# Kernel tuning notes

Hardware: AMD Instinct MI355X
Metric: run time of the kernel (lower is better)

## Reference

```python
import jax, jax.numpy as jnp
import numpy as np

# ---- module hyperparams (match init_kwargs) ----
REGIONS_DIMS = [0, 1, 2, 4, 9, 16]
ALL_DIM = sum(REGIONS_DIMS)          # 32
NUM_REGIONS = len(REGIONS_DIMS)      # 6
FIELD_NUM = 32
VOCAB = 200000
BATCH = 8192
TEMPERATURE = 1.0
EPS = 1e-5                            # torch BatchNorm1d default eps


def _build_region_mask():
    """Replicates init_variables(): row 0 is all-zero (drop-feature region),
    rows 1..R-1 are disjoint consecutive segments of sizes REGIONS_DIMS[1:]."""
    mask = np.zeros((NUM_REGIONS, ALL_DIM), dtype=np.float32)
    dims_pre_sum = [0] + [sum(REGIONS_DIMS[1:i]) for i in range(2, NUM_REGIONS)]
    for r, (pre, dim) in enumerate(zip(dims_pre_sum, REGIONS_DIMS[1:]), start=1):
        mask[r, pre:pre + dim] = 1.0
    return jnp.asarray(mask)


def setup_inputs() -> dict:
    key = jax.random.key(0)
    k_ids, k_emb, k_w = jax.random.split(key, 3)
    input_ids = jax.random.randint(k_ids, (BATCH, FIELD_NUM), 0, VOCAB, dtype=jnp.int64)
    # torch.nn.init.uniform_(a=-0.05, b=0.05)
    emb_table = jax.random.uniform(k_emb, (VOCAB, ALL_DIM), dtype=jnp.float32,
                                   minval=-0.05, maxval=0.05)
    # xavier_uniform on [F, R, 1]: bound = sqrt(6/(R+1))
    bound = float(np.sqrt(6.0 / (NUM_REGIONS + 1)))
    field_region_weights = jax.random.uniform(
        k_w, (FIELD_NUM, NUM_REGIONS, 1), dtype=jnp.float32, minval=-bound, maxval=bound)
    return {
        "input_ids": input_ids,
        "emb_table": emb_table,
        "field_region_weights": field_region_weights,
        "region_mask": _build_region_mask(),
    }


def reference(input_ids, emb_table, field_region_weights, region_mask):
    # Embedding gather: [B, F, D]
    emb = emb_table[input_ids]
    # BatchNorm1d(field_num, affine=False), training mode: per-field stats over (batch, D),
    # biased variance (torch normalizes with biased var).
    mean = jnp.mean(emb, axis=(0, 2), keepdims=True)
    var = jnp.var(emb, axis=(0, 2), keepdims=True)
    x = (emb - mean) * jax.lax.rsqrt(var + EPS)
    # softmax over regions: [F, R]
    w = jax.nn.softmax(field_region_weights[..., 0] / TEMPERATURE, axis=1)
    # sum_r w[f,r] * mask[r,d] -> per-(field, dim) scale; equivalent to the original's
    # broadcast-to-[B,F,R,D], multiply, and sum over R, without the big intermediate.
    coef = jnp.einsum('fr,rd->fd', w, region_mask)
    return x * coef[None, :, :]
```

## Files before the change

kernel.cpp:

```cpp
#include <hip/hip_runtime.h>
#include <math.h>

#define BATCH    8192
#define FIELDS   32
#define DIM      32
#define NREG     6
#define EPS      1e-5f
#define NBLKA    4096
#define PBASE    64
#define SCALE_F  (PBASE + 64 * NBLKA)
#define BIAS_F   (SCALE_F + FIELDS * DIM)


__global__ __launch_bounds__(256) void irazor_stage_stats_kernel(
        const int*   __restrict__ ids,
        const float* __restrict__ table,
        float*       __restrict__ ws,
        float*       __restrict__ out) {
    const int t   = threadIdx.x;
    const int blk = blockIdx.x;
    const int f   = t >> 3;
    const int vec = t & 7;

    float4* __restrict__ out4 = reinterpret_cast<float4*>(out);
    float s = 0.f, sq = 0.f;
    #pragma unroll
    for (int i = 0; i < 2; ++i) {
        const int id = ids[(blk * 2 + i) * FIELDS + f];
        const float4 v = *reinterpret_cast<const float4*>(
            table + (size_t)id * DIM + vec * 4);
        out4[(size_t)blk * 512 + (size_t)i * 256 + t] = v;
        s  += v.x + v.y + v.z + v.w;
        sq += v.x * v.x + v.y * v.y + v.z * v.z + v.w * v.w;
    }

    #pragma unroll
    for (int off = 1; off < 8; off <<= 1) {
        s  += __shfl_xor(s, off);
        sq += __shfl_xor(sq, off);
    }
    if (vec == 0) {
        ws[PBASE + f * NBLKA + blk]        = s;
        ws[PBASE + (32 + f) * NBLKA + blk] = sq;
    }
}

__global__ __launch_bounds__(256) void irazor_finalize_kernel(
        const float* __restrict__ frw,
        const float* __restrict__ mask,
        float*       __restrict__ ws) {
    const int fld = blockIdx.x;
    const int t   = threadIdx.x;

    const float* __restrict__ ps = ws + PBASE + (size_t)fld * NBLKA;
    const float* __restrict__ pq = ws + PBASE + (size_t)(32 + fld) * NBLKA;
    float a = 0.f, b = 0.f;
    #pragma unroll
    for (int i = 0; i < NBLKA / 256; ++i) {
        a += ps[i * 256 + t];
        b += pq[i * 256 + t];
    }
    #pragma unroll
    for (int off = 1; off < 64; off <<= 1) {
        a += __shfl_xor(a, off);
        b += __shfl_xor(b, off);
    }
    __shared__ float ls[4], lq[4];
    const int wave = t >> 6;
    if ((t & 63) == 0) { ls[wave] = a; lq[wave] = b; }
    __syncthreads();
    const float S  = ls[0] + ls[1] + ls[2] + ls[3];
    const float SQ = lq[0] + lq[1] + lq[2] + lq[3];

    if (t < DIM) {
        const float invN = 1.f / (float)(BATCH * DIM);
        const float mean = S * invN;
        const float var  = SQ * invN - mean * mean;
        const float istd = rsqrtf(var + EPS);

        float w[NREG]; float m = -1e30f;
        #pragma unroll
        for (int r = 0; r < NREG; ++r) { w[r] = frw[fld * NREG + r]; m = fmaxf(m, w[r]); }
        float ssum = 0.f;
        #pragma unroll
        for (int r = 0; r < NREG; ++r) { w[r] = __expf(w[r] - m); ssum += w[r]; }
        float c = 0.f;
        #pragma unroll
        for (int r = 0; r < NREG; ++r) c += w[r] * mask[r * DIM + t];
        c /= ssum;

        const float sc = istd * c;
        ws[SCALE_F + fld * DIM + t] = sc;
        ws[BIAS_F  + fld * DIM + t] = -mean * sc;
    }
}

__global__ __launch_bounds__(256) void irazor_apply_kernel(
        const float* __restrict__ ws,
        float*       __restrict__ out) {
    const int t   = threadIdx.x;
    const int blk = blockIdx.x;
    const int f   = t >> 3;
    const int vec = t & 7;

    const float4 sc = *reinterpret_cast<const float4*>(ws + SCALE_F + f * DIM + vec * 4);
    const float4 bi = *reinterpret_cast<const float4*>(ws + BIAS_F  + f * DIM + vec * 4);

    float4* __restrict__ out4 = reinterpret_cast<float4*>(out);
    #pragma unroll
    for (int i = 0; i < 2; ++i) {
        const size_t idx = (size_t)blk * 512 + (size_t)i * 256 + t;
        float4 v = out4[idx];
        float4 o;
        o.x = fmaf(v.x, sc.x, bi.x);
        o.y = fmaf(v.y, sc.y, bi.y);
        o.z = fmaf(v.z, sc.z, bi.z);
        o.w = fmaf(v.w, sc.w, bi.w);
        out4[idx] = o;
    }
}

extern "C" void kernel_launch(void* const* d_in, const int* in_sizes, int n_in,
                              void* d_out, int out_size, void* d_ws, size_t ws_size,
                              hipStream_t stream) {
    const int*   ids   = (const int*)d_in[0];
    const float* table = (const float*)d_in[1];
    const float* frw   = (const float*)d_in[2];
    const float* mask  = (const float*)d_in[3];
    float*       out   = (float*)d_out;
    float*       ws    = (float*)d_ws;

    irazor_stage_stats_kernel<<<NBLKA, 256, 0, stream>>>(ids, table, ws, out);
    irazor_finalize_kernel<<<FIELDS, 256, 0, stream>>>(frw, mask, ws);
    irazor_apply_kernel<<<NBLKA, 256, 0, stream>>>(ws, out);
}
```

Baseline: 105.6 us.

## Compute per-row table stats, then gather stats per id and fuse gather into apply

Field statistics were computed by gathering embeddings into the output buffer, and a second pass then read that buffer back and rewrote it. Now a streaming pass computes the sum and sum of squares of every table row, and a small kernel gathers those two scalars per id to form the per-field partials. The final kernel gathers embeddings straight from the table and writes the normalized output once, so the read-modify-write round trip over the output is gone. In exchange the whole table is read once and there is one extra kernel launch.

```diff
diff --git a/kernel.cpp b/kernel.cpp
--- a/kernel.cpp
+++ b/kernel.cpp
@@ -6,42 +6,68 @@
 #define DIM      32
 #define NREG     6
 #define EPS      1e-5f
-#define NBLKA    4096
+#define NBLK2    256
+#define NBLK4    4096
+#define VOCAB_N  200000
+
 #define PBASE    64
-#define SCALE_F  (PBASE + 64 * NBLKA)
+#define SCALE_F  (PBASE + 2 * FIELDS * NBLK2)
 #define BIAS_F   (SCALE_F + FIELDS * DIM)
+#define RS_F     (BIAS_F + FIELDS * DIM)
+#define RQ_F     (RS_F + VOCAB_N)
 
-
-__global__ __launch_bounds__(256) void irazor_stage_stats_kernel(
-        const int*   __restrict__ ids,
+__global__ __launch_bounds__(256) void irazor_rowstats_kernel(
         const float* __restrict__ table,
         float*       __restrict__ ws,
-        float*       __restrict__ out) {
+        int vocab) {
     const int t   = threadIdx.x;
-    const int blk = blockIdx.x;
-    const int f   = t >> 3;
+    const int r   = blockIdx.x * 32 + (t >> 3);
     const int vec = t & 7;
+    if (r >= vocab) return;
 
-    float4* __restrict__ out4 = reinterpret_cast<float4*>(out);
-    float s = 0.f, sq = 0.f;
-    #pragma unroll
-    for (int i = 0; i < 2; ++i) {
-        const int id = ids[(blk * 2 + i) * FIELDS + f];
-        const float4 v = *reinterpret_cast<const float4*>(
-            table + (size_t)id * DIM + vec * 4);
-        out4[(size_t)blk * 512 + (size_t)i * 256 + t] = v;
-        s  += v.x + v.y + v.z + v.w;
-        sq += v.x * v.x + v.y * v.y + v.z * v.z + v.w * v.w;
-    }
-
+    const float4 v = *reinterpret_cast<const float4*>(
+        table + (size_t)r * DIM + vec * 4);
+    float s  = v.x + v.y + v.z + v.w;
+    float sq = v.x * v.x + v.y * v.y + v.z * v.z + v.w * v.w;
     #pragma unroll
     for (int off = 1; off < 8; off <<= 1) {
         s  += __shfl_xor(s, off);
         sq += __shfl_xor(sq, off);
     }
     if (vec == 0) {
-        ws[PBASE + f * NBLKA + blk]        = s;
-        ws[PBASE + (32 + f) * NBLKA + blk] = sq;
+        ws[RS_F + r] = s;
+        ws[RQ_F + r] = sq;
+    }
+}
+
+__global__ __launch_bounds__(256) void irazor_fieldstats_kernel(
+        const int*   __restrict__ ids,
+        float*       __restrict__ ws) {
+    const int t    = threadIdx.x;
+    const int blk  = blockIdx.x;
+    const int lane = t & 63;
+    const int wave = t >> 6;
+
+    float s = 0.f, sq = 0.f;
+    #pragma unroll
+    for (int i = 0; i < 4; ++i) {
+        const int id = ids[blk * 1024 + i * 256 + t];
+        s  += ws[RS_F + id];
+        sq += ws[RQ_F + id];
+    }
+    s  += __shfl_xor(s, 32);
+    sq += __shfl_xor(sq, 32);
+
+    __shared__ float sm[2][4][32];
+    if (lane < 32) { sm[0][wave][lane] = s; sm[1][wave][lane] = sq; }
+    __syncthreads();
+    if (t < 32) {
+        ws[PBASE + t * NBLK2 + blk] =
+            sm[0][0][t] + sm[0][1][t] + sm[0][2][t] + sm[0][3][t];
+    } else if (t < 64) {
+        const int f = t - 32;
+        ws[PBASE + 8192 + f * NBLK2 + blk] =
+            sm[1][0][f] + sm[1][1][f] + sm[1][2][f] + sm[1][3][f];
     }
 }
 
@@ -52,14 +78,8 @@
     const int fld = blockIdx.x;
     const int t   = threadIdx.x;
 
-    const float* __restrict__ ps = ws + PBASE + (size_t)fld * NBLKA;
-    const float* __restrict__ pq = ws + PBASE + (size_t)(32 + fld) * NBLKA;
-    float a = 0.f, b = 0.f;
-    #pragma unroll
-    for (int i = 0; i < NBLKA / 256; ++i) {
-        a += ps[i * 256 + t];
-        b += pq[i * 256 + t];
-    }
+    float a = ws[PBASE + fld * NBLK2 + t];
+    float b = ws[PBASE + 8192 + fld * NBLK2 + t];
     #pragma unroll
     for (int off = 1; off < 64; off <<= 1) {
         a += __shfl_xor(a, off);
@@ -95,7 +115,9 @@
     }
 }
 
-__global__ __launch_bounds__(256) void irazor_apply_kernel(
+__global__ __launch_bounds__(256) void irazor_out_kernel(
+        const int*   __restrict__ ids,
+        const float* __restrict__ table,
         const float* __restrict__ ws,
         float*       __restrict__ out) {
     const int t   = threadIdx.x;
@@ -109,14 +131,15 @@
     float4* __restrict__ out4 = reinterpret_cast<float4*>(out);
     #pragma unroll
     for (int i = 0; i < 2; ++i) {
-        const size_t idx = (size_t)blk * 512 + (size_t)i * 256 + t;
-        float4 v = out4[idx];
+        const int id = ids[(blk * 2 + i) * FIELDS + f];
+        const float4 v = *reinterpret_cast<const float4*>(
+            table + (size_t)id * DIM + vec * 4);
         float4 o;
         o.x = fmaf(v.x, sc.x, bi.x);
         o.y = fmaf(v.y, sc.y, bi.y);
         o.z = fmaf(v.z, sc.z, bi.z);
         o.w = fmaf(v.w, sc.w, bi.w);
-        out4[idx] = o;
+        out4[(size_t)blk * 512 + (size_t)i * 256 + t] = o;
     }
 }
 
@@ -130,7 +153,10 @@
     float*       out   = (float*)d_out;
     float*       ws    = (float*)d_ws;
 
-    irazor_stage_stats_kernel<<<NBLKA, 256, 0, stream>>>(ids, table, ws, out);
+    const int vocab = in_sizes[1] / DIM;
+
+    irazor_rowstats_kernel<<<(vocab + 31) / 32, 256, 0, stream>>>(table, ws, vocab);
+    irazor_fieldstats_kernel<<<NBLK2, 256, 0, stream>>>(ids, ws);
     irazor_finalize_kernel<<<FIELDS, 256, 0, stream>>>(frw, mask, ws);
-    irazor_apply_kernel<<<NBLKA, 256, 0, stream>>>(ws, out);
+    irazor_out_kernel<<<NBLK4, 256, 0, stream>>>(ids, table, ws, out);
 }
```

Measured after the change: 99.75 us. -5.5%, faster.
